# Kernel optimization log

Measured on AMD Instinct MI355X. Metric: run time of the kernel, lower is better.

## Reference

```python
import jax, jax.numpy as jnp
import numpy as np

N_HEAD = 16
HEAD_SIZE = 64

def setup_inputs() -> dict:
    key = jax.random.key(0)
    ks = jax.random.split(key, 5)
    B, T, C = 2, 2048, 1024
    s = 0.02
    return {
        "x": jax.random.normal(ks[0], (B, T, C), dtype=jnp.float32),
        "We": jax.random.normal(ks[1], (3 * C, C), dtype=jnp.float32) * s,
        "be": jax.random.normal(ks[2], (3 * C,), dtype=jnp.float32) * s,
        "Wp": jax.random.normal(ks[3], (C, C), dtype=jnp.float32) * s,
        "bp": jax.random.normal(ks[4], (C,), dtype=jnp.float32) * s,
    }

def reference(x, We, be, Wp, bp):
    B, T, C = x.shape
    H, D = N_HEAD, HEAD_SIZE
    qkv = x @ We.T + be                      # [B,T,3C]
    q, k, v = jnp.split(qkv, 3, axis=-1)
    # [B,H,T,D]
    q = q.reshape(B, T, H, D).transpose(0, 2, 1, 3)
    k = k.reshape(B, T, H, D).transpose(0, 2, 1, 3)
    v = v.reshape(B, T, H, D).transpose(0, 2, 1, 3)
    scale = 1.0 / jnp.sqrt(jnp.asarray(D, dtype=x.dtype))
    att = jnp.einsum('bhqd,bhkd->bhqk', q, k) * scale
    causal = jnp.tril(jnp.ones((T, T), dtype=bool))
    att = jnp.where(causal, att, -jnp.inf)
    att = jax.nn.softmax(att, axis=-1)
    y = jnp.einsum('bhqk,bhkd->bhqd', att, v)   # [B,H,T,D]
    y = y.transpose(0, 2, 1, 3).reshape(B, T, C)
    return y @ Wp.T + bp
```

## Files before the change

kernel.cpp:

```cpp
#include <hip/hip_runtime.h>
#include <hip/hip_bf16.h>
#include <stdint.h>
#include <stddef.h>

typedef short s8v __attribute__((ext_vector_type(8)));
typedef float f4v __attribute__((ext_vector_type(4)));

__device__ inline float b2f(short s) {
    union { unsigned u; float f; } x;
    x.u = ((unsigned)(unsigned short)s) << 16;
    return x.f;
}
__device__ inline short f2b(float f) {
    union { float f; unsigned u; } x;
    x.f = f;
    unsigned r = x.u + 0x7FFF + ((x.u >> 16) & 1);
    return (short)(r >> 16);
}

__device__ __forceinline__ void gl16(const short* g, short* l) {
    __builtin_amdgcn_global_load_lds(
        (const __attribute__((address_space(1))) void*)g,
        (__attribute__((address_space(3))) void*)l,
        16, 0, 0);
}

__global__ void detect_dtype(const unsigned* __restrict__ x, int* __restrict__ flag)
{
    int hit = 0;
    for (int i = threadIdx.x; i < 1024; i += 64) {
        unsigned lo = x[i] & 0xFFFFu;
        unsigned e = (lo >> 7) & 0xFFu;
        if (e >= 0x8Au) hit = 1;
    }
    unsigned long long any = __ballot(hit != 0);
    if (threadIdx.x == 0) *flag = (any != 0ull) ? 1 : 0;
}

__global__ __launch_bounds__(256) void convert_bf16(
    const void* s0, short* d0, size_t c0,
    const void* s1, short* d1, size_t c1,
    const void* s2, short* d2, size_t c2,
    const void* s3, short* d3, size_t c3,
    const void* s4, short* d4, size_t c4,
    const int* __restrict__ flagp)
{
    const bool f32 = (*flagp != 0);
    const void* srcs[5] = {s0, s1, s2, s3, s4};
    short* dsts[5] = {d0, d1, d2, d3, d4};
    size_t cnts[5] = {c0, c1, c2, c3, c4};
    size_t total = c0 + c1 + c2 + c3 + c4;
    size_t stride = (size_t)gridDim.x * blockDim.x;
    for (size_t c = (size_t)blockIdx.x * blockDim.x + threadIdx.x; c < total; c += stride) {
        size_t r = c; int s = 0;
        while (r >= cnts[s]) { r -= cnts[s]; s++; }
        short* d = dsts[s] + r * 8;
        if (f32) {
            const float* p = (const float*)srcs[s] + r * 8;
            f4v a = *(const f4v*)p;
            f4v b = *(const f4v*)(p + 4);
            s8v v;
            v[0] = f2b(a[0]); v[1] = f2b(a[1]); v[2] = f2b(a[2]); v[3] = f2b(a[3]);
            v[4] = f2b(b[0]); v[5] = f2b(b[1]); v[6] = f2b(b[2]); v[7] = f2b(b[3]);
            *(s8v*)d = v;
        } else {
            *(s8v*)d = *(const s8v*)((const short*)srcs[s] + r * 8);
        }
    }
}

#define BM 128
#define BN 128
#define BKK 64

template<int QKV>
__global__ __launch_bounds__(256) void gemm_bt_bias(
    const short* __restrict__ A,
    const short* __restrict__ B,
    const short* __restrict__ bias,
    void* __restrict__ C,
    short* __restrict__ vT,
    int M, int N, int K, int ldc,
    const int* __restrict__ flagp, int oDyn)
{
    const bool of32 = oDyn && (*flagp != 0);

    __shared__ __align__(16) short smem[QKV ? (128 * 136) : (BM + BN) * BKK];
    short* sA = smem;
    short* sB = smem + BM * BKK;

    const int tid  = threadIdx.x;
    const int lane = tid & 63;
    const int w    = tid >> 6;
    const int wm   = (w >> 1) * 64;
    const int wn   = (w & 1) * 64;
    const int quad = lane >> 4;
    const int l16  = lane & 15;

    const int m0 = blockIdx.y * BM;
    const int n0 = blockIdx.x * BN;

    f4v acc[4][4];
    const f4v vzero = {0.0f, 0.0f, 0.0f, 0.0f};
#pragma unroll
    for (int i = 0; i < 4; i++)
#pragma unroll
        for (int j = 0; j < 4; j++) acc[i][j] = vzero;

    for (int k0 = 0; k0 < K; k0 += BKK) {
        __syncthreads();
#pragma unroll
        for (int i = 0; i < 4; i++) {
            int c  = i * 256 + tid;
            int r  = c >> 3, kk = (c & 7) * 8;
            int cb = i * 256 + (tid & 192);
            gl16(A + (size_t)(m0 + r) * K + k0 + kk, sA + cb * 8);
            gl16(B + (size_t)(n0 + r) * K + k0 + kk, sB + cb * 8);
        }
        __syncthreads();
#pragma unroll
        for (int s = 0; s < 2; s++) {
            s8v af[4], bf[4];
#pragma unroll
            for (int t = 0; t < 4; t++)
                af[t] = *(const s8v*)(sA + (wm + t * 16 + l16) * BKK + s * 32 + quad * 8);
#pragma unroll
            for (int t = 0; t < 4; t++)
                bf[t] = *(const s8v*)(sB + (wn + t * 16 + l16) * BKK + s * 32 + quad * 8);
#pragma unroll
            for (int mt = 0; mt < 4; mt++)
#pragma unroll
                for (int nt = 0; nt < 4; nt++)
                    acc[mt][nt] = __builtin_amdgcn_mfma_f32_16x16x32_bf16(
                        af[mt], bf[nt], acc[mt][nt], 0, 0, 0);
        }
    }

    if (QKV && n0 >= 2048) {
        __syncthreads();
#pragma unroll
        for (int nt = 0; nt < 4; nt++) {
            int nl = wn + nt * 16 + l16;
            float bv = b2f(bias[n0 + nl]);
#pragma unroll
            for (int mt = 0; mt < 4; mt++)
#pragma unroll
                for (int r = 0; r < 4; r++) {
                    int ml = wm + mt * 16 + quad * 4 + r;
                    smem[nl * 136 + ml] = f2b(acc[mt][nt][r] + bv);
                }
        }
        __syncthreads();
        int nl = tid >> 1, half = tid & 1;
        int n = n0 + nl;
        int h = (n - 2048) >> 6, d = n & 63;
        int bq = m0 >> 11;
        short* dst = vT + (((size_t)(bq * 16 + h)) * 64 + d) * 2048 + (m0 & 2047) + half * 64;
        const short* src = smem + nl * 136 + half * 64;
#pragma unroll
        for (int j = 0; j < 8; j++)
            *(s8v*)(dst + j * 8) = *(const s8v*)(src + j * 8);
    } else {
#pragma unroll
        for (int nt = 0; nt < 4; nt++) {
            int n = n0 + wn + nt * 16 + l16;
            float bv = b2f(bias[n]);
#pragma unroll
            for (int mt = 0; mt < 4; mt++) {
#pragma unroll
                for (int r = 0; r < 4; r++) {
                    int m = m0 + wm + mt * 16 + quad * 4 + r;
                    float v = acc[mt][nt][r] + bv;
                    if (of32) ((float*)C)[(size_t)m * ldc + n] = v;
                    else      ((short*)C)[(size_t)m * ldc + n] = f2b(v);
                }
            }
        }
    }
}

#define LP 72

__global__ __launch_bounds__(256) void attn_flash(
    const short* __restrict__ qk,
    const short* __restrict__ vt,
    short* __restrict__ y)
{
    const int T = 2048, LDQ = 2048;
    __shared__ __align__(16) short sK[64 * LP];
    __shared__ __align__(16) short sVT[64 * LP];
    __shared__ __align__(16) short sP[4][16 * LP];

    const int tid  = threadIdx.x;
    const int lane = tid & 63;
    const int w    = tid >> 6;
    const int quad = lane >> 4;
    const int l16  = lane & 15;

    const int bx = blockIdx.x;
    const int qt = 31 - (bx >> 5);
    const int bh = bx & 31;
    const int b  = bh >> 4;
    const int h  = bh & 15;

    const size_t qkbase = (size_t)b * T * LDQ;
    const short* Kbase  = qk + qkbase + 1024 + h * 64;
    const short* Vbase  = vt + (size_t)bh * 64 * 2048;

    s8v qf[2];
    {
        int qrow = qt * 64 + w * 16 + l16;
        const short* qp = qk + qkbase + (size_t)qrow * LDQ + h * 64 + quad * 8;
        qf[0] = *(const s8v*)(qp);
        qf[1] = *(const s8v*)(qp + 32);
    }

    const f4v vzero = {0.0f, 0.0f, 0.0f, 0.0f};
    f4v o[4];
#pragma unroll
    for (int i = 0; i < 4; i++) o[i] = vzero;
    float lsum[4] = {0.0f, 0.0f, 0.0f, 0.0f};

    for (int kt = 0; kt <= qt; kt++) {
        __syncthreads();
#pragma unroll
        for (int i = 0; i < 2; i++) {
            int c = i * 256 + tid;
            int r = c >> 3, dd = (c & 7) * 8;
            s8v kv = *(const s8v*)(Kbase + (size_t)(kt * 64 + r) * LDQ + dd);
            s8v vv = *(const s8v*)(Vbase + (size_t)r * 2048 + kt * 64 + dd);
            *(s8v*)(sK  + r * LP + dd) = kv;
            *(s8v*)(sVT + r * LP + dd) = vv;
        }
        __syncthreads();

        f4v sacc[4];
#pragma unroll
        for (int nt = 0; nt < 4; nt++) {
            sacc[nt] = vzero;
            s8v kf0 = *(const s8v*)(sK + (nt * 16 + l16) * LP + quad * 8);
            s8v kf1 = *(const s8v*)(sK + (nt * 16 + l16) * LP + 32 + quad * 8);
            sacc[nt] = __builtin_amdgcn_mfma_f32_16x16x32_bf16(qf[0], kf0, sacc[nt], 0, 0, 0);
            sacc[nt] = __builtin_amdgcn_mfma_f32_16x16x32_bf16(qf[1], kf1, sacc[nt], 0, 0, 0);
        }

        short* pp = sP[w];
        const bool diag = (kt == qt);
#pragma unroll
        for (int nt = 0; nt < 4; nt++) {
#pragma unroll
            for (int r = 0; r < 4; r++) {
                float p = __expf(sacc[nt][r] * 0.125f);
                if (diag) {
                    int q = w * 16 + quad * 4 + r;
                    int k = nt * 16 + l16;
                    if (k > q) p = 0.0f;
                }
                lsum[r] += p;
                pp[(quad * 4 + r) * LP + nt * 16 + l16] = f2b(p);
            }
        }
        __syncthreads();

        s8v pf0 = *(const s8v*)(pp + l16 * LP + quad * 8);
        s8v pf1 = *(const s8v*)(pp + l16 * LP + 32 + quad * 8);
#pragma unroll
        for (int dt = 0; dt < 4; dt++) {
            s8v vf0 = *(const s8v*)(sVT + (dt * 16 + l16) * LP + quad * 8);
            s8v vf1 = *(const s8v*)(sVT + (dt * 16 + l16) * LP + 32 + quad * 8);
            o[dt] = __builtin_amdgcn_mfma_f32_16x16x32_bf16(pf0, vf0, o[dt], 0, 0, 0);
            o[dt] = __builtin_amdgcn_mfma_f32_16x16x32_bf16(pf1, vf1, o[dt], 0, 0, 0);
        }
    }

#pragma unroll
    for (int r = 0; r < 4; r++) {
        float s = lsum[r];
        s += __shfl_xor(s, 1, 64);
        s += __shfl_xor(s, 2, 64);
        s += __shfl_xor(s, 4, 64);
        s += __shfl_xor(s, 8, 64);
        lsum[r] = 1.0f / s;
    }
#pragma unroll
    for (int dt = 0; dt < 4; dt++)
#pragma unroll
        for (int r = 0; r < 4; r++) {
            int qrow = qt * 64 + w * 16 + quad * 4 + r;
            int d = dt * 16 + l16;
            y[((size_t)b * T + qrow) * 1024 + h * 64 + d] = f2b(o[dt][r] * lsum[r]);
        }
}

extern "C" void kernel_launch(void* const* d_in, const int* in_sizes, int n_in,
                              void* d_out, int out_size, void* d_ws, size_t ws_size,
                              hipStream_t stream)
{
    int*   flag = (int*)d_ws;
    short* qk   = (short*)((char*)d_ws + 16);
    short* vT   = qk  + (size_t)4096 * 2048;
    short* xb   = vT  + (size_t)32 * 64 * 2048;
    short* Web  = xb  + (size_t)4096 * 1024;
    short* Wpb  = Web + (size_t)3072 * 1024;
    short* beb  = Wpb + (size_t)1024 * 1024;
    short* bpb  = beb + 3072;
    short* y    = xb;

    detect_dtype<<<1, 64, 0, stream>>>((const unsigned*)d_in[0], flag);

    convert_bf16<<<dim3(4098), 256, 0, stream>>>(
        d_in[0], xb,  (size_t)4096 * 1024 / 8,
        d_in[1], Web, (size_t)3072 * 1024 / 8,
        d_in[2], beb, (size_t)3072 / 8,
        d_in[3], Wpb, (size_t)1024 * 1024 / 8,
        d_in[4], bpb, (size_t)1024 / 8,
        flag);

    gemm_bt_bias<1><<<dim3(3072 / BN, 4096 / BM), 256, 0, stream>>>(
        xb, Web, beb, qk, vT, 4096, 3072, 1024, 2048, flag, 0);

    attn_flash<<<dim3(1024), 256, 0, stream>>>(qk, vT, y);

    gemm_bt_bias<0><<<dim3(1024 / BN, 4096 / BM), 256, 0, stream>>>(
        y, Wpb, bpb, d_out, nullptr, 4096, 1024, 1024, 1024, flag, 1);
}
```

Before: 228.4 us.

## Double attention query tile per block and narrow output-projection GEMM tile

The attention kernel now handles 128 query rows per block, with each wave owning 32 rows, so every K/V tile loaded into shared memory is reused by twice as many queries. The grid is halved to 512 blocks and the causal mask is applied to the last two key tiles. The output projection GEMM is templated to use a 64-wide N tile, doubling its block count to 512 for better CU occupancy. Risks: fewer attention blocks with more register pressure, and the softmax still has no max subtraction, as before.

Result: slower. 249.3 us (+9.2%).

```diff
diff --git a/kernel.cpp b/kernel.cpp
--- a/kernel.cpp
+++ b/kernel.cpp
@@ -70,10 +70,9 @@
 }
 
 #define BM 128
-#define BN 128
 #define BKK 64
 
-template<int QKV>
+template<int QKV, int TBN>
 __global__ __launch_bounds__(256) void gemm_bt_bias(
     const short* __restrict__ A,
     const short* __restrict__ B,
@@ -84,8 +83,9 @@
     const int* __restrict__ flagp, int oDyn)
 {
     const bool of32 = oDyn && (*flagp != 0);
-
-    __shared__ __align__(16) short smem[QKV ? (128 * 136) : (BM + BN) * BKK];
+    const int NT = TBN / 32;
+
+    __shared__ __align__(16) short smem[QKV ? (128 * 136) : (BM + TBN) * BKK];
     short* sA = smem;
     short* sB = smem + BM * BKK;
 
@@ -93,19 +93,19 @@
     const int lane = tid & 63;
     const int w    = tid >> 6;
     const int wm   = (w >> 1) * 64;
-    const int wn   = (w & 1) * 64;
+    const int wn   = (w & 1) * (TBN / 2);
     const int quad = lane >> 4;
     const int l16  = lane & 15;
 
     const int m0 = blockIdx.y * BM;
-    const int n0 = blockIdx.x * BN;
-
-    f4v acc[4][4];
+    const int n0 = blockIdx.x * TBN;
+
+    f4v acc[4][NT];
     const f4v vzero = {0.0f, 0.0f, 0.0f, 0.0f};
 #pragma unroll
     for (int i = 0; i < 4; i++)
 #pragma unroll
-        for (int j = 0; j < 4; j++) acc[i][j] = vzero;
+        for (int j = 0; j < NT; j++) acc[i][j] = vzero;
 
     for (int k0 = 0; k0 < K; k0 += BKK) {
         __syncthreads();
@@ -115,22 +115,23 @@
             int r  = c >> 3, kk = (c & 7) * 8;
             int cb = i * 256 + (tid & 192);
             gl16(A + (size_t)(m0 + r) * K + k0 + kk, sA + cb * 8);
-            gl16(B + (size_t)(n0 + r) * K + k0 + kk, sB + cb * 8);
+            if (i < TBN / 32)
+                gl16(B + (size_t)(n0 + r) * K + k0 + kk, sB + cb * 8);
         }
         __syncthreads();
 #pragma unroll
         for (int s = 0; s < 2; s++) {
-            s8v af[4], bf[4];
+            s8v af[4], bf[NT];
 #pragma unroll
             for (int t = 0; t < 4; t++)
                 af[t] = *(const s8v*)(sA + (wm + t * 16 + l16) * BKK + s * 32 + quad * 8);
 #pragma unroll
-            for (int t = 0; t < 4; t++)
+            for (int t = 0; t < NT; t++)
                 bf[t] = *(const s8v*)(sB + (wn + t * 16 + l16) * BKK + s * 32 + quad * 8);
 #pragma unroll
             for (int mt = 0; mt < 4; mt++)
 #pragma unroll
-                for (int nt = 0; nt < 4; nt++)
+                for (int nt = 0; nt < NT; nt++)
                     acc[mt][nt] = __builtin_amdgcn_mfma_f32_16x16x32_bf16(
                         af[mt], bf[nt], acc[mt][nt], 0, 0, 0);
         }
@@ -139,7 +140,7 @@
     if (QKV && n0 >= 2048) {
         __syncthreads();
 #pragma unroll
-        for (int nt = 0; nt < 4; nt++) {
+        for (int nt = 0; nt < NT; nt++) {
             int nl = wn + nt * 16 + l16;
             float bv = b2f(bias[n0 + nl]);
 #pragma unroll
@@ -162,7 +163,7 @@
             *(s8v*)(dst + j * 8) = *(const s8v*)(src + j * 8);
     } else {
 #pragma unroll
-        for (int nt = 0; nt < 4; nt++) {
+        for (int nt = 0; nt < NT; nt++) {
             int n = n0 + wn + nt * 16 + l16;
             float bv = b2f(bias[n]);
 #pragma unroll
@@ -189,7 +190,7 @@
     const int T = 2048, LDQ = 2048;
     __shared__ __align__(16) short sK[64 * LP];
     __shared__ __align__(16) short sVT[64 * LP];
-    __shared__ __align__(16) short sP[4][16 * LP];
+    __shared__ __align__(16) short sP[4][32 * LP];
 
     const int tid  = threadIdx.x;
     const int lane = tid & 63;
@@ -198,7 +199,7 @@
     const int l16  = lane & 15;
 
     const int bx = blockIdx.x;
-    const int qt = 31 - (bx >> 5);
+    const int qt = 15 - (bx >> 5);
     const int bh = bx & 31;
     const int b  = bh >> 4;
     const int h  = bh & 15;
@@ -207,21 +208,25 @@
     const short* Kbase  = qk + qkbase + 1024 + h * 64;
     const short* Vbase  = vt + (size_t)bh * 64 * 2048;
 
-    s8v qf[2];
-    {
-        int qrow = qt * 64 + w * 16 + l16;
+    s8v qf[2][2];
+#pragma unroll
+    for (int mt = 0; mt < 2; mt++) {
+        int qrow = qt * 128 + w * 32 + mt * 16 + l16;
         const short* qp = qk + qkbase + (size_t)qrow * LDQ + h * 64 + quad * 8;
-        qf[0] = *(const s8v*)(qp);
-        qf[1] = *(const s8v*)(qp + 32);
+        qf[mt][0] = *(const s8v*)(qp);
+        qf[mt][1] = *(const s8v*)(qp + 32);
     }
 
     const f4v vzero = {0.0f, 0.0f, 0.0f, 0.0f};
-    f4v o[4];
-#pragma unroll
-    for (int i = 0; i < 4; i++) o[i] = vzero;
-    float lsum[4] = {0.0f, 0.0f, 0.0f, 0.0f};
-
-    for (int kt = 0; kt <= qt; kt++) {
+    f4v o[2][4];
+#pragma unroll
+    for (int mt = 0; mt < 2; mt++)
+#pragma unroll
+        for (int i = 0; i < 4; i++) o[mt][i] = vzero;
+    float lsum[2][4] = {{0, 0, 0, 0}, {0, 0, 0, 0}};
+
+    const int ktmax = 2 * qt + 1;
+    for (int kt = 0; kt <= ktmax; kt++) {
         __syncthreads();
 #pragma unroll
         for (int i = 0; i < 2; i++) {
@@ -234,62 +239,78 @@
         }
         __syncthreads();
 
-        f4v sacc[4];
+        f4v sacc[2][4];
 #pragma unroll
         for (int nt = 0; nt < 4; nt++) {
-            sacc[nt] = vzero;
             s8v kf0 = *(const s8v*)(sK + (nt * 16 + l16) * LP + quad * 8);
             s8v kf1 = *(const s8v*)(sK + (nt * 16 + l16) * LP + 32 + quad * 8);
-            sacc[nt] = __builtin_amdgcn_mfma_f32_16x16x32_bf16(qf[0], kf0, sacc[nt], 0, 0, 0);
-            sacc[nt] = __builtin_amdgcn_mfma_f32_16x16x32_bf16(qf[1], kf1, sacc[nt], 0, 0, 0);
+#pragma unroll
+            for (int mt = 0; mt < 2; mt++) {
+                f4v t = vzero;
+                t = __builtin_amdgcn_mfma_f32_16x16x32_bf16(qf[mt][0], kf0, t, 0, 0, 0);
+                t = __builtin_amdgcn_mfma_f32_16x16x32_bf16(qf[mt][1], kf1, t, 0, 0, 0);
+                sacc[mt][nt] = t;
+            }
         }
 
         short* pp = sP[w];
-        const bool diag = (kt == qt);
-#pragma unroll
-        for (int nt = 0; nt < 4; nt++) {
-#pragma unroll
-            for (int r = 0; r < 4; r++) {
-                float p = __expf(sacc[nt][r] * 0.125f);
-                if (diag) {
-                    int q = w * 16 + quad * 4 + r;
-                    int k = nt * 16 + l16;
-                    if (k > q) p = 0.0f;
+        const bool diag = (kt >= 2 * qt);
+        const int kbase = (kt - 2 * qt) * 64;
+#pragma unroll
+        for (int mt = 0; mt < 2; mt++)
+#pragma unroll
+            for (int nt = 0; nt < 4; nt++)
+#pragma unroll
+                for (int r = 0; r < 4; r++) {
+                    float p = __expf(sacc[mt][nt][r] * 0.125f);
+                    if (diag) {
+                        int q = w * 32 + mt * 16 + quad * 4 + r;
+                        int k = kbase + nt * 16 + l16;
+                        if (k > q) p = 0.0f;
+                    }
+                    lsum[mt][r] += p;
+                    pp[(mt * 16 + quad * 4 + r) * LP + nt * 16 + l16] = f2b(p);
                 }
-                lsum[r] += p;
-                pp[(quad * 4 + r) * LP + nt * 16 + l16] = f2b(p);
-            }
-        }
-        __syncthreads();
-
-        s8v pf0 = *(const s8v*)(pp + l16 * LP + quad * 8);
-        s8v pf1 = *(const s8v*)(pp + l16 * LP + 32 + quad * 8);
+        __syncthreads();
+
+        s8v pf[2][2];
+#pragma unroll
+        for (int mt = 0; mt < 2; mt++) {
+            pf[mt][0] = *(const s8v*)(pp + (mt * 16 + l16) * LP + quad * 8);
+            pf[mt][1] = *(const s8v*)(pp + (mt * 16 + l16) * LP + 32 + quad * 8);
+        }
 #pragma unroll
         for (int dt = 0; dt < 4; dt++) {
             s8v vf0 = *(const s8v*)(sVT + (dt * 16 + l16) * LP + quad * 8);
             s8v vf1 = *(const s8v*)(sVT + (dt * 16 + l16) * LP + 32 + quad * 8);
-            o[dt] = __builtin_amdgcn_mfma_f32_16x16x32_bf16(pf0, vf0, o[dt], 0, 0, 0);
-            o[dt] = __builtin_amdgcn_mfma_f32_16x16x32_bf16(pf1, vf1, o[dt], 0, 0, 0);
-        }
-    }
-
-#pragma unroll
-    for (int r = 0; r < 4; r++) {
-        float s = lsum[r];
-        s += __shfl_xor(s, 1, 64);
-        s += __shfl_xor(s, 2, 64);
-        s += __shfl_xor(s, 4, 64);
-        s += __shfl_xor(s, 8, 64);
-        lsum[r] = 1.0f / s;
-    }
-#pragma unroll
-    for (int dt = 0; dt < 4; dt++)
+#pragma unroll
+            for (int mt = 0; mt < 2; mt++) {
+                o[mt][dt] = __builtin_amdgcn_mfma_f32_16x16x32_bf16(pf[mt][0], vf0, o[mt][dt], 0, 0, 0);
+                o[mt][dt] = __builtin_amdgcn_mfma_f32_16x16x32_bf16(pf[mt][1], vf1, o[mt][dt], 0, 0, 0);
+            }
+        }
+    }
+
+#pragma unroll
+    for (int mt = 0; mt < 2; mt++) {
 #pragma unroll
         for (int r = 0; r < 4; r++) {
-            int qrow = qt * 64 + w * 16 + quad * 4 + r;
-            int d = dt * 16 + l16;
-            y[((size_t)b * T + qrow) * 1024 + h * 64 + d] = f2b(o[dt][r] * lsum[r]);
-        }
+            float s = lsum[mt][r];
+            s += __shfl_xor(s, 1, 64);
+            s += __shfl_xor(s, 2, 64);
+            s += __shfl_xor(s, 4, 64);
+            s += __shfl_xor(s, 8, 64);
+            lsum[mt][r] = 1.0f / s;
+        }
+#pragma unroll
+        for (int dt = 0; dt < 4; dt++)
+#pragma unroll
+            for (int r = 0; r < 4; r++) {
+                int qrow = qt * 128 + w * 32 + mt * 16 + quad * 4 + r;
+                int d = dt * 16 + l16;
+                y[((size_t)b * T + qrow) * 1024 + h * 64 + d] = f2b(o[mt][dt][r] * lsum[mt][r]);
+            }
+    }
 }
 
 extern "C" void kernel_launch(void* const* d_in, const int* in_sizes, int n_in,
@@ -316,11 +337,11 @@
         d_in[4], bpb, (size_t)1024 / 8,
         flag);
 
-    gemm_bt_bias<1><<<dim3(3072 / BN, 4096 / BM), 256, 0, stream>>>(
+    gemm_bt_bias<1, 128><<<dim3(3072 / 128, 4096 / BM), 256, 0, stream>>>(
         xb, Web, beb, qk, vT, 4096, 3072, 1024, 2048, flag, 0);
 
-    attn_flash<<<dim3(1024), 256, 0, stream>>>(qk, vT, y);
-
-    gemm_bt_bias<0><<<dim3(1024 / BN, 4096 / BM), 256, 0, stream>>>(
+    attn_flash<<<dim3(512), 256, 0, stream>>>(qk, vT, y);
+
+    gemm_bt_bias<0, 64><<<dim3(1024 / 64, 4096 / BM), 256, 0, stream>>>(
         y, Wpb, bpb, d_out, nullptr, 4096, 1024, 1024, 1024, flag, 1);
 }
```
